# Kernel optimization log

Measured on AMD Instinct MI355X. Metric: run time of the kernel, lower is better.

The kernel has to match this reference:

```python
import jax, jax.numpy as jnp
import numpy as np

B, S, D = 4, 2048, 1024
E, K, I = 8, 2, 3072
LBL_COEF, RZL_COEF = 0.01, 0.001
STD = 0.02


def setup_inputs() -> dict:
    key = jax.random.key(0)
    kx, kr, k1, k2, k3 = jax.random.split(key, 5)
    x = jax.random.normal(kx, (B, S, D), dtype=jnp.float32)
    router_w = STD * jax.random.truncated_normal(kr, -3, 3, (D, E), dtype=jnp.float32)
    w1 = STD * jax.random.truncated_normal(k1, -3, 3, (E, D, I), dtype=jnp.float32)
    w2 = STD * jax.random.truncated_normal(k2, -3, 3, (E, D, I), dtype=jnp.float32)
    w3 = STD * jax.random.truncated_normal(k3, -3, 3, (E, I, D), dtype=jnp.float32)
    return {"x": x, "router_w": router_w, "w1": w1, "w2": w2, "w3": w3}


def reference(x, router_w, w1, w2, w3):
    b, s, d = x.shape
    T = b * s
    x_flat = x.reshape(T, d)                                   # [T, D]

    # --- router ---
    router_logits = jnp.einsum("td,de->te", x_flat, router_w)  # [T, E]
    router_probs = jax.nn.softmax(router_logits, axis=-1)
    _, topk_idx = jax.lax.top_k(router_logits, K)              # [T, K] int32
    topk_weights = jnp.take_along_axis(router_probs, topk_idx, axis=-1)
    topk_weights = topk_weights / jnp.sum(topk_weights, axis=-1, keepdims=True)

    # --- permute: sort expanded token copies by expert id ---
    topk_idx_flat = topk_idx.reshape(T * K)                    # [TR]
    sort_idx = jnp.argsort(topk_idx_flat)                      # [TR]
    x_repeat_sort = jnp.take(x_flat, sort_idx // K, axis=0)    # [TR, D]
    group_sizes = jnp.bincount(topk_idx_flat, length=E).astype(jnp.int32)

    # --- grouped GEMM SwiGLU ---
    w1_out = jax.lax.ragged_dot(x_repeat_sort, w1, group_sizes)  # [TR, I]
    w2_out = jax.lax.ragged_dot(x_repeat_sort, w2, group_sizes)  # [TR, I]
    gated = jax.nn.silu(w1_out) * w2_out
    out_repeat_sort = jax.lax.ragged_dot(gated, w3, group_sizes)  # [TR, D]

    # --- unpermute + weighted combine ---
    inv_sort_idx = jnp.argsort(sort_idx)
    out_repeat = jnp.take(out_repeat_sort, inv_sort_idx, axis=0).reshape(T, K, d)
    out_flat = jnp.sum(out_repeat * topk_weights[..., None], axis=1)  # [T, D]
    out = out_flat.reshape(b, s, d)

    # --- aux losses ---
    gs_f = group_sizes.astype(jnp.float32)
    expert_loads = gs_f / jnp.sum(gs_f)                        # [E]
    f = expert_loads * (E / K)
    p = jnp.mean(router_probs.astype(jnp.float32), axis=0)
    load_balancing_loss = jnp.float32(LBL_COEF) * jnp.sum(f * p)
    z = jax.scipy.special.logsumexp(router_logits.astype(jnp.float32), axis=-1)
    router_z_loss = jnp.float32(RZL_COEF) * jnp.mean(z ** 2)

    return out, expert_loads, load_balancing_loss, router_z_loss
```

## Files before the change

kernel.cpp:

```cpp
#include <hip/hip_runtime.h>
#include <stdint.h>

#define TK   8192
#define DD   1024
#define EE   8
#define II   3072
#define TR   16384
#define TRP  (TR + 128)
#define MAXTILES 136

typedef float  f32x4  __attribute__((ext_vector_type(4)));
typedef __bf16 bf16x8 __attribute__((ext_vector_type(8)));
typedef short  s16x8  __attribute__((ext_vector_type(8)));

__device__ __forceinline__ unsigned short f2bf(float f) {
    union { float f; unsigned u; } v; v.f = f;
    unsigned r = v.u + 0x7fff + ((v.u >> 16) & 1);
    return (unsigned short)(r >> 16);
}
__device__ __forceinline__ float bf2f(unsigned short b) {
    union { unsigned u; float f; } v; v.u = ((unsigned)b) << 16;
    return v.f;
}
__device__ __forceinline__ void async16(const void* g, void* l) {
    __builtin_amdgcn_global_load_lds(
        (const __attribute__((address_space(1))) unsigned int*)g,
        (__attribute__((address_space(3))) unsigned int*)l, 16, 0, 0);
}

__global__ void init_kernel(int* p) {
    int i = threadIdx.x;
#pragma unroll
    for (int j = 0; j < 4; ++j) p[j * 256 + i] = 0;
}

__global__ __launch_bounds__(256) void transpose_conv(const float* __restrict__ src,
                                                      unsigned short* __restrict__ dst,
                                                      int R, int C) {
    __shared__ float tile[64][65];
    int b = blockIdx.z, rt = blockIdx.y, ct = blockIdx.x;
    int tid = threadIdx.x;
    const float* s = src + (size_t)b * R * C + (size_t)(rt * 64) * C + ct * 64;
    unsigned short* d = dst + (size_t)b * R * C + (size_t)(ct * 64) * R + rt * 64;
#pragma unroll
    for (int i = tid; i < 4096; i += 256) {
        int r = i >> 6, c = i & 63;
        tile[r][c] = s[(size_t)r * C + c];
    }
    __syncthreads();
#pragma unroll
    for (int i = tid; i < 1024; i += 256) {
        int dr = i >> 4, dq = i & 15;
        ushort4 v;
        v.x = f2bf(tile[dq * 4 + 0][dr]);
        v.y = f2bf(tile[dq * 4 + 1][dr]);
        v.z = f2bf(tile[dq * 4 + 2][dr]);
        v.w = f2bf(tile[dq * 4 + 3][dr]);
        *(ushort4*)&d[(size_t)dr * R + dq * 4] = v;
    }
}

__global__ __launch_bounds__(256) void router_kernel(const float* __restrict__ x,
                                                     const float* __restrict__ rw,
                                                     int* __restrict__ counts,
                                                     float* __restrict__ probsum,
                                                     float* __restrict__ z2sum,
                                                     int* __restrict__ tk_idx,
                                                     float* __restrict__ tk_w) {
    __shared__ float lrw[8][1024];
    __shared__ float pacc[8];
    __shared__ float zacc;
    __shared__ int   cacc[8];
    int tid = threadIdx.x;
    for (int i = tid; i < 8192; i += 256) lrw[i & 7][i >> 3] = rw[i];
    if (tid < 8) { pacc[tid] = 0.f; cacc[tid] = 0; }
    if (tid == 0) zacc = 0.f;
    __syncthreads();
    int lane = tid & 63, wv = tid >> 6;
    for (int t = blockIdx.x * 4 + wv; t < TK; t += 1024) {
        float part[8];
#pragma unroll
        for (int e = 0; e < 8; ++e) part[e] = 0.f;
        const float* xr = x + ((size_t)t << 10);
        for (int j = 0; j < 16; ++j) {
            float xv = xr[j * 64 + lane];
#pragma unroll
            for (int e = 0; e < 8; ++e) part[e] += xv * lrw[e][j * 64 + lane];
        }
#pragma unroll
        for (int e = 0; e < 8; ++e) {
            float v = part[e];
            v += __shfl_xor(v, 32); v += __shfl_xor(v, 16); v += __shfl_xor(v, 8);
            v += __shfl_xor(v, 4);  v += __shfl_xor(v, 2);  v += __shfl_xor(v, 1);
            part[e] = v;
        }
        if (lane == 0) {
            float m = part[0];
#pragma unroll
            for (int e = 1; e < 8; ++e) m = fmaxf(m, part[e]);
            float pe[8]; float se = 0.f;
#pragma unroll
            for (int e = 0; e < 8; ++e) { pe[e] = __expf(part[e] - m); se += pe[e]; }
            float inv = 1.0f / se;
            int i0 = 0; float v0 = part[0];
#pragma unroll
            for (int e = 1; e < 8; ++e) if (part[e] > v0) { v0 = part[e]; i0 = e; }
            int i1 = -1; float v1 = -1e30f;
#pragma unroll
            for (int e = 0; e < 8; ++e) if (e != i0 && part[e] > v1) { v1 = part[e]; i1 = e; }
            float p0 = pe[i0] * inv, p1 = pe[i1] * inv;
            float wn = 1.0f / (p0 + p1);
            tk_idx[t * 2 + 0] = i0; tk_idx[t * 2 + 1] = i1;
            tk_w[t * 2 + 0] = p0 * wn; tk_w[t * 2 + 1] = p1 * wn;
            float z = __logf(se) + m;
            atomicAdd(&zacc, z * z);
#pragma unroll
            for (int e = 0; e < 8; ++e) atomicAdd(&pacc[e], pe[e] * inv);
            atomicAdd(&cacc[i0], 1);
            atomicAdd(&cacc[i1], 1);
        }
    }
    __syncthreads();
    if (tid < 8) { atomicAdd(&counts[tid], cacc[tid]); atomicAdd(&probsum[tid], pacc[tid]); }
    if (tid == 0) atomicAdd(z2sum, zacc);
}

__global__ void finalize_kernel(const int* __restrict__ counts, const float* __restrict__ probsum,
                                const float* __restrict__ z2sum, int* __restrict__ base,
                                int* __restrict__ cursor, int* __restrict__ tile_e,
                                int* __restrict__ tile_r0, int* __restrict__ tile_rc,
                                int* __restrict__ num_tiles, float* __restrict__ out_aux) {
    if (threadIdx.x != 0) return;
    int b = 0; float lbl = 0.f;
    for (int e = 0; e < 8; ++e) {
        int c = counts[e];
        base[e] = b; cursor[e] = b;
        float load = (float)c / 16384.0f;
        out_aux[e] = load;
        lbl += (load * 4.0f) * (probsum[e] / 8192.0f);
        b += c;
    }
    out_aux[8] = 0.01f * lbl;
    out_aux[9] = 0.001f * (*z2sum / 8192.0f);
    int nt = 0;
    for (int e = 0; e < 8; ++e) {
        int c = counts[e];
        int r0 = base[e];
        for (int i = 0; i < c; i += 128) {
            tile_e[nt] = e; tile_r0[nt] = r0 + i;
            int rem = c - i;
            tile_rc[nt] = rem < 128 ? rem : 128;
            ++nt;
        }
    }
    *num_tiles = nt;
}

__global__ __launch_bounds__(256) void scatter_kernel(const int* __restrict__ tk_idx,
                                                      const float* __restrict__ tk_w,
                                                      int* __restrict__ cursor,
                                                      int* __restrict__ row_token,
                                                      float* __restrict__ row_w,
                                                      int* __restrict__ pos) {
    __shared__ int hist[8];
    __shared__ int lbase[8];
    int tid = threadIdx.x;
    if (tid < 8) hist[tid] = 0;
    __syncthreads();
    int start = blockIdx.x * 2048;
#pragma unroll
    for (int j = 0; j < 8; ++j) atomicAdd(&hist[tk_idx[start + j * 256 + tid]], 1);
    __syncthreads();
    if (tid < 8) lbase[tid] = atomicAdd(&cursor[tid], hist[tid]);
    __syncthreads();
    if (tid < 8) hist[tid] = 0;
    __syncthreads();
#pragma unroll
    for (int j = 0; j < 8; ++j) {
        int idx = start + j * 256 + tid;
        int e = tk_idx[idx];
        int r = lbase[e] + atomicAdd(&hist[e], 1);
        row_token[r] = idx >> 1;
        row_w[r] = tk_w[idx];
        pos[idx] = r;
    }
}

__global__ __launch_bounds__(256) void gather_kernel(const float* __restrict__ x,
                                                     const int* __restrict__ row_token,
                                                     unsigned short* __restrict__ xp) {
    int idx = blockIdx.x * 256 + threadIdx.x;
    int r = idx >> 7, j = idx & 127;
    int t = row_token[r];
    const float4* s = (const float4*)(x + ((size_t)t << 10) + (j << 3));
    float4 v0 = s[0], v1 = s[1];
    s16x8 o;
    o[0] = (short)f2bf(v0.x); o[1] = (short)f2bf(v0.y);
    o[2] = (short)f2bf(v0.z); o[3] = (short)f2bf(v0.w);
    o[4] = (short)f2bf(v1.x); o[5] = (short)f2bf(v1.y);
    o[6] = (short)f2bf(v1.z); o[7] = (short)f2bf(v1.w);
    *(s16x8*)(xp + ((size_t)r << 10) + (j << 3)) = o;
}

__global__ __launch_bounds__(256, 2) void gemm1_kernel(const short* __restrict__ Xp,
                                                       const short* __restrict__ W1t,
                                                       const short* __restrict__ W2t,
                                                       unsigned short* __restrict__ H,
                                                       const int* __restrict__ tile_e,
                                                       const int* __restrict__ tile_r0,
                                                       const int* __restrict__ tile_rc,
                                                       const int* __restrict__ num_tiles) {
    int mt = blockIdx.y;
    if (mt >= *num_tiles) return;
    int e = tile_e[mt], m0 = tile_r0[mt], rows = tile_rc[mt];
    int n0 = blockIdx.x << 7;

    __shared__ __align__(16) short As[128 * 64];
    __shared__ __align__(16) short B1s[128 * 64];
    __shared__ __align__(16) short B2s[128 * 64];

    int tid = threadIdx.x, lane = tid & 63, wv = tid >> 6;
    int wm = wv >> 1, wn = wv & 1;

    f32x4 z4 = {0.f, 0.f, 0.f, 0.f};
    f32x4 acc1[4][4], acc2[4][4];
#pragma unroll
    for (int a = 0; a < 4; ++a)
#pragma unroll
        for (int b = 0; b < 4; ++b) { acc1[a][b] = z4; acc2[a][b] = z4; }

    int swz = (lane & 7) ^ ((lane >> 3) & 7);
    const short* ab  = Xp  + (size_t)(m0 + wv * 32 + (lane >> 3)) * 1024 + swz * 8;
    const short* b1b = W1t + ((size_t)e * 3072 + n0 + wv * 32 + (lane >> 3)) * 1024 + swz * 8;
    const short* b2b = W2t + ((size_t)e * 3072 + n0 + wv * 32 + (lane >> 3)) * 1024 + swz * 8;
    short* asw = As  + wv * 32 * 64;
    short* b1w = B1s + wv * 32 * 64;
    short* b2w = B2s + wv * 32 * 64;

    for (int k0 = 0; k0 < 1024; k0 += 64) {
#pragma unroll
        for (int i = 0; i < 4; ++i) {
            async16(ab  + (size_t)i * 8 * 1024 + k0, asw + i * 8 * 64);
            async16(b1b + (size_t)i * 8 * 1024 + k0, b1w + i * 8 * 64);
            async16(b2b + (size_t)i * 8 * 1024 + k0, b2w + i * 8 * 64);
        }
        __syncthreads();
#pragma unroll
        for (int kk = 0; kk < 2; ++kk) {
            bf16x8 af[4];
#pragma unroll
            for (int mi = 0; mi < 4; ++mi) {
                int ar = wm * 64 + mi * 16 + (lane & 15);
                int ac = (kk * 4 + (lane >> 4)) ^ (ar & 7);
                af[mi] = *(const bf16x8*)&As[ar * 64 + ac * 8];
            }
#pragma unroll
            for (int ni = 0; ni < 4; ++ni) {
                int br = wn * 64 + ni * 16 + (lane & 15);
                int bc = (kk * 4 + (lane >> 4)) ^ (br & 7);
                bf16x8 b1 = *(const bf16x8*)&B1s[br * 64 + bc * 8];
                bf16x8 b2 = *(const bf16x8*)&B2s[br * 64 + bc * 8];
#pragma unroll
                for (int mi = 0; mi < 4; ++mi) {
                    acc1[mi][ni] = __builtin_amdgcn_mfma_f32_16x16x32_bf16(af[mi], b1, acc1[mi][ni], 0, 0, 0);
                    acc2[mi][ni] = __builtin_amdgcn_mfma_f32_16x16x32_bf16(af[mi], b2, acc2[mi][ni], 0, 0, 0);
                }
            }
        }
        __syncthreads();
    }
#pragma unroll
    for (int mi = 0; mi < 4; ++mi) {
#pragma unroll
        for (int i = 0; i < 4; ++i) {
            int rl = wm * 64 + mi * 16 + (lane >> 4) * 4 + i;
            if (rl < rows) {
                size_t rowoff = (size_t)(m0 + rl) * 3072 + n0;
#pragma unroll
                for (int ni = 0; ni < 4; ++ni) {
                    int cl = wn * 64 + ni * 16 + (lane & 15);
                    float c1 = acc1[mi][ni][i];
                    float c2 = acc2[mi][ni][i];
                    float hv = c1 * c2 / (1.0f + __expf(-c1));
                    H[rowoff + cl] = f2bf(hv);
                }
            }
        }
    }
}

__global__ __launch_bounds__(256, 2) void gemm2_kernel(const short* __restrict__ Hs,
                                                       const short* __restrict__ W3t,
                                                       const float* __restrict__ row_w,
                                                       unsigned short* __restrict__ OR,
                                                       const int* __restrict__ tile_e,
                                                       const int* __restrict__ tile_r0,
                                                       const int* __restrict__ tile_rc,
                                                       const int* __restrict__ num_tiles) {
    int mt = blockIdx.y;
    if (mt >= *num_tiles) return;
    int e = tile_e[mt], m0 = tile_r0[mt], rows = tile_rc[mt];
    int n0 = blockIdx.x << 7;

    __shared__ __align__(16) short As[128 * 64];
    __shared__ __align__(16) short Bs[128 * 64];

    int tid = threadIdx.x, lane = tid & 63, wv = tid >> 6;
    int wm = wv >> 1, wn = wv & 1;

    f32x4 z4 = {0.f, 0.f, 0.f, 0.f};
    f32x4 acc[4][4];
#pragma unroll
    for (int a = 0; a < 4; ++a)
#pragma unroll
        for (int b = 0; b < 4; ++b) acc[a][b] = z4;

    int swz = (lane & 7) ^ ((lane >> 3) & 7);
    const short* ab = Hs  + (size_t)(m0 + wv * 32 + (lane >> 3)) * 3072 + swz * 8;
    const short* bb = W3t + ((size_t)e * 1024 + n0 + wv * 32 + (lane >> 3)) * 3072 + swz * 8;
    short* asw = As + wv * 32 * 64;
    short* bsw = Bs + wv * 32 * 64;

    for (int k0 = 0; k0 < 3072; k0 += 64) {
#pragma unroll
        for (int i = 0; i < 4; ++i) {
            async16(ab + (size_t)i * 8 * 3072 + k0, asw + i * 8 * 64);
            async16(bb + (size_t)i * 8 * 3072 + k0, bsw + i * 8 * 64);
        }
        __syncthreads();
#pragma unroll
        for (int kk = 0; kk < 2; ++kk) {
            bf16x8 af[4];
#pragma unroll
            for (int mi = 0; mi < 4; ++mi) {
                int ar = wm * 64 + mi * 16 + (lane & 15);
                int ac = (kk * 4 + (lane >> 4)) ^ (ar & 7);
                af[mi] = *(const bf16x8*)&As[ar * 64 + ac * 8];
            }
#pragma unroll
            for (int ni = 0; ni < 4; ++ni) {
                int br = wn * 64 + ni * 16 + (lane & 15);
                int bc = (kk * 4 + (lane >> 4)) ^ (br & 7);
                bf16x8 bfr = *(const bf16x8*)&Bs[br * 64 + bc * 8];
#pragma unroll
                for (int mi = 0; mi < 4; ++mi)
                    acc[mi][ni] = __builtin_amdgcn_mfma_f32_16x16x32_bf16(af[mi], bfr, acc[mi][ni], 0, 0, 0);
            }
        }
        __syncthreads();
    }
#pragma unroll
    for (int mi = 0; mi < 4; ++mi) {
#pragma unroll
        for (int i = 0; i < 4; ++i) {
            int rl = wm * 64 + mi * 16 + (lane >> 4) * 4 + i;
            if (rl < rows) {
                float sc = row_w[m0 + rl];
                size_t rowoff = (size_t)(m0 + rl) * 1024 + n0;
#pragma unroll
                for (int ni = 0; ni < 4; ++ni) {
                    int cl = wn * 64 + ni * 16 + (lane & 15);
                    OR[rowoff + cl] = f2bf(acc[mi][ni][i] * sc);
                }
            }
        }
    }
}

__global__ __launch_bounds__(256) void combine_kernel(const unsigned short* __restrict__ rows,
                                                      const int* __restrict__ pos,
                                                      float* __restrict__ out) {
    int idx = blockIdx.x * 256 + threadIdx.x;
    int t = idx >> 7, j = idx & 127;
    int p0 = pos[t * 2 + 0], p1 = pos[t * 2 + 1];
    s16x8 a = *(const s16x8*)(rows + ((size_t)p0 << 10) + (j << 3));
    s16x8 b = *(const s16x8*)(rows + ((size_t)p1 << 10) + (j << 3));
    float4 o0, o1;
    o0.x = bf2f((unsigned short)a[0]) + bf2f((unsigned short)b[0]);
    o0.y = bf2f((unsigned short)a[1]) + bf2f((unsigned short)b[1]);
    o0.z = bf2f((unsigned short)a[2]) + bf2f((unsigned short)b[2]);
    o0.w = bf2f((unsigned short)a[3]) + bf2f((unsigned short)b[3]);
    o1.x = bf2f((unsigned short)a[4]) + bf2f((unsigned short)b[4]);
    o1.y = bf2f((unsigned short)a[5]) + bf2f((unsigned short)b[5]);
    o1.z = bf2f((unsigned short)a[6]) + bf2f((unsigned short)b[6]);
    o1.w = bf2f((unsigned short)a[7]) + bf2f((unsigned short)b[7]);
    float* dst = out + ((size_t)t << 10) + (j << 3);
    ((float4*)dst)[0] = o0;
    ((float4*)dst)[1] = o1;
}

extern "C" void kernel_launch(void* const* d_in, const int* in_sizes, int n_in,
                              void* d_out, int out_size, void* d_ws, size_t ws_size,
                              hipStream_t stream) {
    const float* x  = (const float*)d_in[0];
    const float* rw = (const float*)d_in[1];
    const float* w1 = (const float*)d_in[2];
    const float* w2 = (const float*)d_in[3];
    const float* w3 = (const float*)d_in[4];
    float* out = (float*)d_out;
    char* ws = (char*)d_ws;

    int*   counts    = (int*)(ws + 0);
    int*   cursor    = (int*)(ws + 32);
    float* probsum   = (float*)(ws + 64);
    float* z2sum     = (float*)(ws + 96);
    int*   num_tiles = (int*)(ws + 100);
    int*   base      = (int*)(ws + 128);
    int*   tile_e    = (int*)(ws + 256);
    int*   tile_r0   = (int*)(ws + 1024);
    int*   tile_rc   = (int*)(ws + 1792);
    int*   row_token = (int*)(ws + 2560);
    float* row_w     = (float*)(ws + 68096);
    int*   pos       = (int*)(ws + 133632);
    int*   tk_idx    = (int*)(ws + 199168);
    float* tk_w      = (float*)(ws + 264704);
    unsigned short* xp   = (unsigned short*)(ws + 330240);
    unsigned short* w1t  = (unsigned short*)(ws + 34146816);
    unsigned short* w2t  = (unsigned short*)(ws + 84478464);
    unsigned short* w3t  = (unsigned short*)(ws + 134810112);
    unsigned short* h    = (unsigned short*)(ws + 185141760);
    unsigned short* orows= (unsigned short*)(ws + 286591488);

    init_kernel<<<dim3(1), dim3(256), 0, stream>>>((int*)ws);
    transpose_conv<<<dim3(II / 64, DD / 64, EE), dim3(256), 0, stream>>>(w1, w1t, DD, II);
    transpose_conv<<<dim3(II / 64, DD / 64, EE), dim3(256), 0, stream>>>(w2, w2t, DD, II);
    transpose_conv<<<dim3(DD / 64, II / 64, EE), dim3(256), 0, stream>>>(w3, w3t, II, DD);
    router_kernel<<<dim3(256), dim3(256), 0, stream>>>(x, rw, counts, probsum, z2sum, tk_idx, tk_w);
    finalize_kernel<<<dim3(1), dim3(64), 0, stream>>>(counts, probsum, z2sum, base, cursor,
                                                      tile_e, tile_r0, tile_rc, num_tiles,
                                                      out + (size_t)TK * DD);
    scatter_kernel<<<dim3(8), dim3(256), 0, stream>>>(tk_idx, tk_w, cursor, row_token, row_w, pos);
    gather_kernel<<<dim3(TR * DD / 8 / 256), dim3(256), 0, stream>>>(x, row_token, xp);
    gemm1_kernel<<<dim3(II / 128, MAXTILES), dim3(256), 0, stream>>>(
        (const short*)xp, (const short*)w1t, (const short*)w2t, h,
        tile_e, tile_r0, tile_rc, num_tiles);
    gemm2_kernel<<<dim3(DD / 128, MAXTILES), dim3(256), 0, stream>>>(
        (const short*)h, (const short*)w3t, row_w, orows,
        tile_e, tile_r0, tile_rc, num_tiles);
    combine_kernel<<<dim3(TK * DD / 8 / 256), dim3(256), 0, stream>>>(orows, pos, out);
}
```

Measured before the change: 775.5 us.

## Persistent grouped GEMMs, fused weight transpose, parallel finalize and wider scatter

Turns both grouped GEMM kernels into persistent grids of 512 blocks that stride over a flattened (m-tile, n-tile) list, so launches no longer reserve idle blocks for unused tiles. The three weight transpose launches become one kernel with vectorized float4 loads and 8-wide bf16 stores. The tile table in finalize is now built by 256 threads instead of one, and scatter uses 64 blocks instead of 8. The persistent GEMM loop visits tiles in m-major order, which may change L2 reuse of weights, and the scatter now makes more global atomic calls on the cursor.

After: 789.0 us. Within noise of the previous version (+1.7%).

```diff
diff --git a/kernel.cpp b/kernel.cpp
--- a/kernel.cpp
+++ b/kernel.cpp
@@ -8,10 +8,12 @@
 #define TR   16384
 #define TRP  (TR + 128)
 #define MAXTILES 136
+#define PERSIST_BLOCKS 512
 
 typedef float  f32x4  __attribute__((ext_vector_type(4)));
 typedef __bf16 bf16x8 __attribute__((ext_vector_type(8)));
 typedef short  s16x8  __attribute__((ext_vector_type(8)));
+typedef unsigned short u16x8 __attribute__((ext_vector_type(8)));
 
 __device__ __forceinline__ unsigned short f2bf(float f) {
     union { float f; unsigned u; } v; v.f = f;
@@ -34,29 +36,41 @@
     for (int j = 0; j < 4; ++j) p[j * 256 + i] = 0;
 }
 
-__global__ __launch_bounds__(256) void transpose_conv(const float* __restrict__ src,
-                                                      unsigned short* __restrict__ dst,
-                                                      int R, int C) {
+__global__ __launch_bounds__(256) void transpose_all(const float* __restrict__ w1,
+                                                     const float* __restrict__ w2,
+                                                     const float* __restrict__ w3,
+                                                     unsigned short* __restrict__ w1t,
+                                                     unsigned short* __restrict__ w2t,
+                                                     unsigned short* __restrict__ w3t) {
     __shared__ float tile[64][65];
-    int b = blockIdx.z, rt = blockIdx.y, ct = blockIdx.x;
-    int tid = threadIdx.x;
+    int z = blockIdx.y;
+    int which = z >> 3, b = z & 7;
+    const float* src; unsigned short* dst; int R, C;
+    if (which == 0)      { src = w1; dst = w1t; R = DD; C = II; }
+    else if (which == 1) { src = w2; dst = w2t; R = DD; C = II; }
+    else                 { src = w3; dst = w3t; R = II; C = DD; }
+    int ctiles = C >> 6;
+    int ct = blockIdx.x % ctiles, rt = blockIdx.x / ctiles;
     const float* s = src + (size_t)b * R * C + (size_t)(rt * 64) * C + ct * 64;
     unsigned short* d = dst + (size_t)b * R * C + (size_t)(ct * 64) * R + rt * 64;
-#pragma unroll
-    for (int i = tid; i < 4096; i += 256) {
-        int r = i >> 6, c = i & 63;
-        tile[r][c] = s[(size_t)r * C + c];
-    }
-    __syncthreads();
-#pragma unroll
-    for (int i = tid; i < 1024; i += 256) {
-        int dr = i >> 4, dq = i & 15;
-        ushort4 v;
-        v.x = f2bf(tile[dq * 4 + 0][dr]);
-        v.y = f2bf(tile[dq * 4 + 1][dr]);
-        v.z = f2bf(tile[dq * 4 + 2][dr]);
-        v.w = f2bf(tile[dq * 4 + 3][dr]);
-        *(ushort4*)&d[(size_t)dr * R + dq * 4] = v;
+    int tid = threadIdx.x;
+#pragma unroll
+    for (int k = 0; k < 4; ++k) {
+        int j = tid + k * 256;
+        int r = j >> 4, c4 = j & 15;
+        float4 v = *(const float4*)&s[(size_t)r * C + c4 * 4];
+        tile[r][c4 * 4 + 0] = v.x; tile[r][c4 * 4 + 1] = v.y;
+        tile[r][c4 * 4 + 2] = v.z; tile[r][c4 * 4 + 3] = v.w;
+    }
+    __syncthreads();
+#pragma unroll
+    for (int k = 0; k < 2; ++k) {
+        int u = tid + k * 256;
+        int dr = u >> 3, dq = u & 7;
+        u16x8 v;
+#pragma unroll
+        for (int j = 0; j < 8; ++j) v[j] = f2bf(tile[dq * 8 + j][dr]);
+        *(u16x8*)&d[(size_t)dr * R + dq * 8] = v;
     }
 }
 
@@ -125,35 +139,42 @@
     if (tid == 0) atomicAdd(z2sum, zacc);
 }
 
-__global__ void finalize_kernel(const int* __restrict__ counts, const float* __restrict__ probsum,
+__global__ __launch_bounds__(256) void finalize_kernel(const int* __restrict__ counts,
+                                const float* __restrict__ probsum,
                                 const float* __restrict__ z2sum, int* __restrict__ base,
                                 int* __restrict__ cursor, int* __restrict__ tile_e,
                                 int* __restrict__ tile_r0, int* __restrict__ tile_rc,
                                 int* __restrict__ num_tiles, float* __restrict__ out_aux) {
-    if (threadIdx.x != 0) return;
-    int b = 0; float lbl = 0.f;
-    for (int e = 0; e < 8; ++e) {
-        int c = counts[e];
-        base[e] = b; cursor[e] = b;
-        float load = (float)c / 16384.0f;
-        out_aux[e] = load;
-        lbl += (load * 4.0f) * (probsum[e] / 8192.0f);
-        b += c;
-    }
-    out_aux[8] = 0.01f * lbl;
-    out_aux[9] = 0.001f * (*z2sum / 8192.0f);
-    int nt = 0;
-    for (int e = 0; e < 8; ++e) {
-        int c = counts[e];
-        int r0 = base[e];
-        for (int i = 0; i < c; i += 128) {
-            tile_e[nt] = e; tile_r0[nt] = r0 + i;
-            int rem = c - i;
-            tile_rc[nt] = rem < 128 ? rem : 128;
-            ++nt;
-        }
-    }
-    *num_tiles = nt;
+    __shared__ int scnt[8], sbase[8], tstart[9];
+    int tid = threadIdx.x;
+    if (tid == 0) {
+        int b = 0, ts = 0; float lbl = 0.f;
+        for (int e = 0; e < 8; ++e) {
+            int c = counts[e];
+            scnt[e] = c; sbase[e] = b; tstart[e] = ts;
+            base[e] = b; cursor[e] = b;
+            float load = (float)c / 16384.0f;
+            out_aux[e] = load;
+            lbl += (load * 4.0f) * (probsum[e] / 8192.0f);
+            b += c; ts += (c + 127) >> 7;
+        }
+        tstart[8] = ts;
+        *num_tiles = ts;
+        out_aux[8] = 0.01f * lbl;
+        out_aux[9] = 0.001f * (*z2sum / 8192.0f);
+    }
+    __syncthreads();
+    int nt = tstart[8];
+    for (int u = tid; u < nt; u += 256) {
+        int e = 0;
+#pragma unroll
+        for (int k = 0; k < 8; ++k) if (u >= tstart[k + 1]) e = k + 1;
+        int i = u - tstart[e];
+        int rem = scnt[e] - (i << 7);
+        tile_e[u] = e;
+        tile_r0[u] = sbase[e] + (i << 7);
+        tile_rc[u] = rem < 128 ? rem : 128;
+    }
 }
 
 __global__ __launch_bounds__(256) void scatter_kernel(const int* __restrict__ tk_idx,
@@ -167,23 +188,18 @@
     int tid = threadIdx.x;
     if (tid < 8) hist[tid] = 0;
     __syncthreads();
-    int start = blockIdx.x * 2048;
-#pragma unroll
-    for (int j = 0; j < 8; ++j) atomicAdd(&hist[tk_idx[start + j * 256 + tid]], 1);
+    int idx = blockIdx.x * 256 + tid;
+    int e = tk_idx[idx];
+    atomicAdd(&hist[e], 1);
     __syncthreads();
     if (tid < 8) lbase[tid] = atomicAdd(&cursor[tid], hist[tid]);
     __syncthreads();
     if (tid < 8) hist[tid] = 0;
     __syncthreads();
-#pragma unroll
-    for (int j = 0; j < 8; ++j) {
-        int idx = start + j * 256 + tid;
-        int e = tk_idx[idx];
-        int r = lbase[e] + atomicAdd(&hist[e], 1);
-        row_token[r] = idx >> 1;
-        row_w[r] = tk_w[idx];
-        pos[idx] = r;
-    }
+    int r = lbase[e] + atomicAdd(&hist[e], 1);
+    row_token[r] = idx >> 1;
+    row_w[r] = tk_w[idx];
+    pos[idx] = r;
 }
 
 __global__ __launch_bounds__(256) void gather_kernel(const float* __restrict__ x,
@@ -210,79 +226,81 @@
                                                        const int* __restrict__ tile_r0,
                                                        const int* __restrict__ tile_rc,
                                                        const int* __restrict__ num_tiles) {
-    int mt = blockIdx.y;
-    if (mt >= *num_tiles) return;
-    int e = tile_e[mt], m0 = tile_r0[mt], rows = tile_rc[mt];
-    int n0 = blockIdx.x << 7;
-
     __shared__ __align__(16) short As[128 * 64];
     __shared__ __align__(16) short B1s[128 * 64];
     __shared__ __align__(16) short B2s[128 * 64];
 
     int tid = threadIdx.x, lane = tid & 63, wv = tid >> 6;
     int wm = wv >> 1, wn = wv & 1;
-
-    f32x4 z4 = {0.f, 0.f, 0.f, 0.f};
-    f32x4 acc1[4][4], acc2[4][4];
-#pragma unroll
-    for (int a = 0; a < 4; ++a)
-#pragma unroll
-        for (int b = 0; b < 4; ++b) { acc1[a][b] = z4; acc2[a][b] = z4; }
-
     int swz = (lane & 7) ^ ((lane >> 3) & 7);
-    const short* ab  = Xp  + (size_t)(m0 + wv * 32 + (lane >> 3)) * 1024 + swz * 8;
-    const short* b1b = W1t + ((size_t)e * 3072 + n0 + wv * 32 + (lane >> 3)) * 1024 + swz * 8;
-    const short* b2b = W2t + ((size_t)e * 3072 + n0 + wv * 32 + (lane >> 3)) * 1024 + swz * 8;
     short* asw = As  + wv * 32 * 64;
     short* b1w = B1s + wv * 32 * 64;
     short* b2w = B2s + wv * 32 * 64;
 
-    for (int k0 = 0; k0 < 1024; k0 += 64) {
-#pragma unroll
-        for (int i = 0; i < 4; ++i) {
-            async16(ab  + (size_t)i * 8 * 1024 + k0, asw + i * 8 * 64);
-            async16(b1b + (size_t)i * 8 * 1024 + k0, b1w + i * 8 * 64);
-            async16(b2b + (size_t)i * 8 * 1024 + k0, b2w + i * 8 * 64);
-        }
-        __syncthreads();
-#pragma unroll
-        for (int kk = 0; kk < 2; ++kk) {
-            bf16x8 af[4];
-#pragma unroll
-            for (int mi = 0; mi < 4; ++mi) {
-                int ar = wm * 64 + mi * 16 + (lane & 15);
-                int ac = (kk * 4 + (lane >> 4)) ^ (ar & 7);
-                af[mi] = *(const bf16x8*)&As[ar * 64 + ac * 8];
-            }
-#pragma unroll
-            for (int ni = 0; ni < 4; ++ni) {
-                int br = wn * 64 + ni * 16 + (lane & 15);
-                int bc = (kk * 4 + (lane >> 4)) ^ (br & 7);
-                bf16x8 b1 = *(const bf16x8*)&B1s[br * 64 + bc * 8];
-                bf16x8 b2 = *(const bf16x8*)&B2s[br * 64 + bc * 8];
+    int total = *num_tiles * 24;
+    for (int t = blockIdx.x; t < total; t += PERSIST_BLOCKS) {
+        int mt = t / 24, ntile = t - mt * 24;
+        int e = tile_e[mt], m0 = tile_r0[mt], rows = tile_rc[mt];
+        int n0 = ntile << 7;
+
+        f32x4 z4 = {0.f, 0.f, 0.f, 0.f};
+        f32x4 acc1[4][4], acc2[4][4];
+#pragma unroll
+        for (int a = 0; a < 4; ++a)
+#pragma unroll
+            for (int b = 0; b < 4; ++b) { acc1[a][b] = z4; acc2[a][b] = z4; }
+
+        const short* ab  = Xp  + (size_t)(m0 + wv * 32 + (lane >> 3)) * 1024 + swz * 8;
+        const short* b1b = W1t + ((size_t)e * 3072 + n0 + wv * 32 + (lane >> 3)) * 1024 + swz * 8;
+        const short* b2b = W2t + ((size_t)e * 3072 + n0 + wv * 32 + (lane >> 3)) * 1024 + swz * 8;
+
+        for (int k0 = 0; k0 < 1024; k0 += 64) {
+#pragma unroll
+            for (int i = 0; i < 4; ++i) {
+                async16(ab  + (size_t)i * 8 * 1024 + k0, asw + i * 8 * 64);
+                async16(b1b + (size_t)i * 8 * 1024 + k0, b1w + i * 8 * 64);
+                async16(b2b + (size_t)i * 8 * 1024 + k0, b2w + i * 8 * 64);
+            }
+            __syncthreads();
+#pragma unroll
+            for (int kk = 0; kk < 2; ++kk) {
+                bf16x8 af[4];
 #pragma unroll
                 for (int mi = 0; mi < 4; ++mi) {
-                    acc1[mi][ni] = __builtin_amdgcn_mfma_f32_16x16x32_bf16(af[mi], b1, acc1[mi][ni], 0, 0, 0);
-                    acc2[mi][ni] = __builtin_amdgcn_mfma_f32_16x16x32_bf16(af[mi], b2, acc2[mi][ni], 0, 0, 0);
-                }
-            }
-        }
-        __syncthreads();
-    }
-#pragma unroll
-    for (int mi = 0; mi < 4; ++mi) {
-#pragma unroll
-        for (int i = 0; i < 4; ++i) {
-            int rl = wm * 64 + mi * 16 + (lane >> 4) * 4 + i;
-            if (rl < rows) {
-                size_t rowoff = (size_t)(m0 + rl) * 3072 + n0;
+                    int ar = wm * 64 + mi * 16 + (lane & 15);
+                    int ac = (kk * 4 + (lane >> 4)) ^ (ar & 7);
+                    af[mi] = *(const bf16x8*)&As[ar * 64 + ac * 8];
+                }
 #pragma unroll
                 for (int ni = 0; ni < 4; ++ni) {
-                    int cl = wn * 64 + ni * 16 + (lane & 15);
-                    float c1 = acc1[mi][ni][i];
-                    float c2 = acc2[mi][ni][i];
-                    float hv = c1 * c2 / (1.0f + __expf(-c1));
-                    H[rowoff + cl] = f2bf(hv);
+                    int br = wn * 64 + ni * 16 + (lane & 15);
+                    int bc = (kk * 4 + (lane >> 4)) ^ (br & 7);
+                    bf16x8 b1 = *(const bf16x8*)&B1s[br * 64 + bc * 8];
+                    bf16x8 b2 = *(const bf16x8*)&B2s[br * 64 + bc * 8];
+#pragma unroll
+                    for (int mi = 0; mi < 4; ++mi) {
+                        acc1[mi][ni] = __builtin_amdgcn_mfma_f32_16x16x32_bf16(af[mi], b1, acc1[mi][ni], 0, 0, 0);
+                        acc2[mi][ni] = __builtin_amdgcn_mfma_f32_16x16x32_bf16(af[mi], b2, acc2[mi][ni], 0, 0, 0);
+                    }
+                }
+            }
+            __syncthreads();
+        }
+#pragma unroll
+        for (int mi = 0; mi < 4; ++mi) {
+#pragma unroll
+            for (int i = 0; i < 4; ++i) {
+                int rl = wm * 64 + mi * 16 + (lane >> 4) * 4 + i;
+                if (rl < rows) {
+                    size_t rowoff = (size_t)(m0 + rl) * 3072 + n0;
+#pragma unroll
+                    for (int ni = 0; ni < 4; ++ni) {
+                        int cl = wn * 64 + ni * 16 + (lane & 15);
+                        float c1 = acc1[mi][ni][i];
+                        float c2 = acc2[mi][ni][i];
+                        float hv = c1 * c2 / (1.0f + __expf(-c1));
+                        H[rowoff + cl] = f2bf(hv);
+                    }
                 }
             }
         }
@@ -297,70 +315,72 @@
                                                        const int* __restrict__ tile_r0,
                                                        const int* __restrict__ tile_rc,
                                                        const int* __restrict__ num_tiles) {
-    int mt = blockIdx.y;
-    if (mt >= *num_tiles) return;
-    int e = tile_e[mt], m0 = tile_r0[mt], rows = tile_rc[mt];
-    int n0 = blockIdx.x << 7;
-
     __shared__ __align__(16) short As[128 * 64];
     __shared__ __align__(16) short Bs[128 * 64];
 
     int tid = threadIdx.x, lane = tid & 63, wv = tid >> 6;
     int wm = wv >> 1, wn = wv & 1;
-
-    f32x4 z4 = {0.f, 0.f, 0.f, 0.f};
-    f32x4 acc[4][4];
-#pragma unroll
-    for (int a = 0; a < 4; ++a)
-#pragma unroll
-        for (int b = 0; b < 4; ++b) acc[a][b] = z4;
-
     int swz = (lane & 7) ^ ((lane >> 3) & 7);
-    const short* ab = Hs  + (size_t)(m0 + wv * 32 + (lane >> 3)) * 3072 + swz * 8;
-    const short* bb = W3t + ((size_t)e * 1024 + n0 + wv * 32 + (lane >> 3)) * 3072 + swz * 8;
     short* asw = As + wv * 32 * 64;
     short* bsw = Bs + wv * 32 * 64;
 
-    for (int k0 = 0; k0 < 3072; k0 += 64) {
-#pragma unroll
-        for (int i = 0; i < 4; ++i) {
-            async16(ab + (size_t)i * 8 * 3072 + k0, asw + i * 8 * 64);
-            async16(bb + (size_t)i * 8 * 3072 + k0, bsw + i * 8 * 64);
-        }
-        __syncthreads();
-#pragma unroll
-        for (int kk = 0; kk < 2; ++kk) {
-            bf16x8 af[4];
-#pragma unroll
-            for (int mi = 0; mi < 4; ++mi) {
-                int ar = wm * 64 + mi * 16 + (lane & 15);
-                int ac = (kk * 4 + (lane >> 4)) ^ (ar & 7);
-                af[mi] = *(const bf16x8*)&As[ar * 64 + ac * 8];
-            }
-#pragma unroll
-            for (int ni = 0; ni < 4; ++ni) {
-                int br = wn * 64 + ni * 16 + (lane & 15);
-                int bc = (kk * 4 + (lane >> 4)) ^ (br & 7);
-                bf16x8 bfr = *(const bf16x8*)&Bs[br * 64 + bc * 8];
-#pragma unroll
-                for (int mi = 0; mi < 4; ++mi)
-                    acc[mi][ni] = __builtin_amdgcn_mfma_f32_16x16x32_bf16(af[mi], bfr, acc[mi][ni], 0, 0, 0);
-            }
-        }
-        __syncthreads();
-    }
-#pragma unroll
-    for (int mi = 0; mi < 4; ++mi) {
-#pragma unroll
-        for (int i = 0; i < 4; ++i) {
-            int rl = wm * 64 + mi * 16 + (lane >> 4) * 4 + i;
-            if (rl < rows) {
-                float sc = row_w[m0 + rl];
-                size_t rowoff = (size_t)(m0 + rl) * 1024 + n0;
+    int total = *num_tiles * 8;
+    for (int t = blockIdx.x; t < total; t += PERSIST_BLOCKS) {
+        int mt = t >> 3, ntile = t & 7;
+        int e = tile_e[mt], m0 = tile_r0[mt], rows = tile_rc[mt];
+        int n0 = ntile << 7;
+
+        f32x4 z4 = {0.f, 0.f, 0.f, 0.f};
+        f32x4 acc[4][4];
+#pragma unroll
+        for (int a = 0; a < 4; ++a)
+#pragma unroll
+            for (int b = 0; b < 4; ++b) acc[a][b] = z4;
+
+        const short* ab = Hs  + (size_t)(m0 + wv * 32 + (lane >> 3)) * 3072 + swz * 8;
+        const short* bb = W3t + ((size_t)e * 1024 + n0 + wv * 32 + (lane >> 3)) * 3072 + swz * 8;
+
+        for (int k0 = 0; k0 < 3072; k0 += 64) {
+#pragma unroll
+            for (int i = 0; i < 4; ++i) {
+                async16(ab + (size_t)i * 8 * 3072 + k0, asw + i * 8 * 64);
+                async16(bb + (size_t)i * 8 * 3072 + k0, bsw + i * 8 * 64);
+            }
+            __syncthreads();
+#pragma unroll
+            for (int kk = 0; kk < 2; ++kk) {
+                bf16x8 af[4];
+#pragma unroll
+                for (int mi = 0; mi < 4; ++mi) {
+                    int ar = wm * 64 + mi * 16 + (lane & 15);
+                    int ac = (kk * 4 + (lane >> 4)) ^ (ar & 7);
+                    af[mi] = *(const bf16x8*)&As[ar * 64 + ac * 8];
+                }
 #pragma unroll
                 for (int ni = 0; ni < 4; ++ni) {
-                    int cl = wn * 64 + ni * 16 + (lane & 15);
-                    OR[rowoff + cl] = f2bf(acc[mi][ni][i] * sc);
+                    int br = wn * 64 + ni * 16 + (lane & 15);
+                    int bc = (kk * 4 + (lane >> 4)) ^ (br & 7);
+                    bf16x8 bfr = *(const bf16x8*)&Bs[br * 64 + bc * 8];
+#pragma unroll
+                    for (int mi = 0; mi < 4; ++mi)
+                        acc[mi][ni] = __builtin_amdgcn_mfma_f32_16x16x32_bf16(af[mi], bfr, acc[mi][ni], 0, 0, 0);
+                }
+            }
+            __syncthreads();
+        }
+#pragma unroll
+        for (int mi = 0; mi < 4; ++mi) {
+#pragma unroll
+            for (int i = 0; i < 4; ++i) {
+                int rl = wm * 64 + mi * 16 + (lane >> 4) * 4 + i;
+                if (rl < rows) {
+                    float sc = row_w[m0 + rl];
+                    size_t rowoff = (size_t)(m0 + rl) * 1024 + n0;
+#pragma unroll
+                    for (int ni = 0; ni < 4; ++ni) {
+                        int cl = wn * 64 + ni * 16 + (lane & 15);
+                        OR[rowoff + cl] = f2bf(acc[mi][ni][i] * sc);
+                    }
                 }
             }
         }
@@ -422,19 +442,17 @@
     unsigned short* orows= (unsigned short*)(ws + 286591488);
 
     init_kernel<<<dim3(1), dim3(256), 0, stream>>>((int*)ws);
-    transpose_conv<<<dim3(II / 64, DD / 64, EE), dim3(256), 0, stream>>>(w1, w1t, DD, II);
-    transpose_conv<<<dim3(II / 64, DD / 64, EE), dim3(256), 0, stream>>>(w2, w2t, DD, II);
-    transpose_conv<<<dim3(DD / 64, II / 64, EE), dim3(256), 0, stream>>>(w3, w3t, II, DD);
+    transpose_all<<<dim3(768, 24), dim3(256), 0, stream>>>(w1, w2, w3, w1t, w2t, w3t);
     router_kernel<<<dim3(256), dim3(256), 0, stream>>>(x, rw, counts, probsum, z2sum, tk_idx, tk_w);
-    finalize_kernel<<<dim3(1), dim3(64), 0, stream>>>(counts, probsum, z2sum, base, cursor,
-                                                      tile_e, tile_r0, tile_rc, num_tiles,
-                                                      out + (size_t)TK * DD);
-    scatter_kernel<<<dim3(8), dim3(256), 0, stream>>>(tk_idx, tk_w, cursor, row_token, row_w, pos);
+    finalize_kernel<<<dim3(1), dim3(256), 0, stream>>>(counts, probsum, z2sum, base, cursor,
+                                                       tile_e, tile_r0, tile_rc, num_tiles,
+                                                       out + (size_t)TK * DD);
+    scatter_kernel<<<dim3(64), dim3(256), 0, stream>>>(tk_idx, tk_w, cursor, row_token, row_w, pos);
     gather_kernel<<<dim3(TR * DD / 8 / 256), dim3(256), 0, stream>>>(x, row_token, xp);
-    gemm1_kernel<<<dim3(II / 128, MAXTILES), dim3(256), 0, stream>>>(
+    gemm1_kernel<<<dim3(PERSIST_BLOCKS), dim3(256), 0, stream>>>(
         (const short*)xp, (const short*)w1t, (const short*)w2t, h,
         tile_e, tile_r0, tile_rc, num_tiles);
-    gemm2_kernel<<<dim3(DD / 128, MAXTILES), dim3(256), 0, stream>>>(
+    gemm2_kernel<<<dim3(PERSIST_BLOCKS), dim3(256), 0, stream>>>(
         (const short*)h, (const short*)w3t, row_w, orows,
         tile_e, tile_r0, tile_rc, num_tiles);
     combine_kernel<<<dim3(TK * DD / 8 / 256), dim3(256), 0, stream>>>(orows, pos, out);
```
